# Kernel tuning notes

Measured on AMD Instinct MI355X. Metric: run time of the kernel, lower is better.

## Reference

```python
import jax, jax.numpy as jnp
import numpy as np

N_NODES = 100000
N_EDGES = 1600000
FEAT = 128
EMB = 32
N_GRAPHS = 512


def gcn_conv(x, W, b, src, dst, deg_inv_sqrt):
    # PyG GCNConv: h = x @ W; propagate with norm = d_i^{-1/2} d_j^{-1/2} over A + I
    h = x @ W  # [N, out]
    norm = deg_inv_sqrt[src] * deg_inv_sqrt[dst]  # [E]
    msg = h[src] * norm[:, None]  # gather + scale
    agg = jax.ops.segment_sum(msg, dst, num_segments=N_NODES)
    # self-loop contribution: norm_ii = d_i^{-1}
    agg = agg + h * (deg_inv_sqrt * deg_inv_sqrt)[:, None]
    return agg + b


def setup_inputs() -> dict:
    key = jax.random.key(0)
    ks = jax.random.split(key, 10)
    x = jax.random.normal(ks[0], (N_NODES, FEAT), dtype=jnp.float32)
    edge_index = jax.random.randint(ks[1], (2, N_EDGES), 0, N_NODES, dtype=jnp.int64)
    batch_index = jnp.sort(jax.random.randint(ks[2], (N_NODES,), 0, N_GRAPHS, dtype=jnp.int64))
    # Glorot-ish init for weights (PyG GCNConv lin has no bias arg here but conv bias exists)
    def glorot(k, fan_in, fan_out):
        s = jnp.sqrt(6.0 / (fan_in + fan_out)).astype(jnp.float32)
        return jax.random.uniform(k, (fan_in, fan_out), jnp.float32, -s, s)
    W1 = glorot(ks[3], FEAT, EMB)
    b1 = jnp.zeros((EMB,), jnp.float32)
    W2 = glorot(ks[4], EMB, EMB)
    b2 = jnp.zeros((EMB,), jnp.float32)
    Wo = glorot(ks[5], EMB, 1)
    bo = jnp.zeros((1,), jnp.float32)
    return {"x": x, "edge_index": edge_index, "batch_index": batch_index,
            "W1": W1, "b1": b1, "W2": W2, "b2": b2, "Wo": Wo, "bo": bo}


def reference(x, edge_index, batch_index, W1, b1, W2, b2, Wo, bo):
    src, dst = edge_index[0], edge_index[1]
    # degree over A + I (edge weights = 1, counted on dst as in PyG)
    deg = jax.ops.segment_sum(jnp.ones((N_EDGES,), x.dtype), dst, num_segments=N_NODES) + 1.0
    deg_inv_sqrt = jax.lax.rsqrt(deg)

    out = jax.nn.relu(gcn_conv(x, W1, b1, src, dst, deg_inv_sqrt))
    out = jax.nn.relu(gcn_conv(out, W2, b2, src, dst, deg_inv_sqrt))

    # global mean pool over graphs
    summed = jax.ops.segment_sum(out, batch_index, num_segments=N_GRAPHS)  # [G, EMB]
    counts = jax.ops.segment_sum(jnp.ones((N_NODES,), x.dtype), batch_index, num_segments=N_GRAPHS)
    pooled = summed / jnp.maximum(counts, 1.0)[:, None]

    return pooled @ Wo + bo  # [G, 1]
```

## Files before the change

### kernel.cpp

```cpp
#include <hip/hip_runtime.h>
#include <hip/hip_fp16.h>

#define N_NODES 100000
#define N_EDGES 1600000
#define N_GRAPHS 512
#define FEAT 128
#define EMB 32
#define ZROW N_NODES
#define NCOPY 64
#define NBKT 500
#define NPB 200
#define CAPB 4096
#define COLCAP 5120
#define ABLK 512
#define EPB 3125
#define NTILE (N_NODES / 16)
#define AGB (N_NODES / 32)

typedef unsigned short u16;
typedef unsigned int u32;
typedef _Float16 f16;
typedef float f32x4 __attribute__((ext_vector_type(4)));
typedef unsigned short u16x4 __attribute__((ext_vector_type(4)));
typedef f16 f16x8 __attribute__((ext_vector_type(8)));

__device__ __forceinline__ float4 h4_to_f4(u16x4 v) {
  union { unsigned int u; __half2 h; } a, b;
  a.u = (unsigned int)v.x | ((unsigned int)v.y << 16);
  b.u = (unsigned int)v.z | ((unsigned int)v.w << 16);
  float2 f0 = __half22float2(a.h);
  float2 f1 = __half22float2(b.h);
  return make_float4(f0.x, f0.y, f1.x, f1.y);
}

__device__ __forceinline__ u16x4 f4_to_h4(float4 f) {
  union { unsigned int u; __half2 h; } a, b;
  a.h = __float22half2_rn(make_float2(f.x, f.y));
  b.h = __float22half2_rn(make_float2(f.z, f.w));
  u16x4 r;
  r.x = (u16)(a.u & 0xffff); r.y = (u16)(a.u >> 16);
  r.z = (u16)(b.u & 0xffff); r.w = (u16)(b.u >> 16);
  return r;
}

__device__ __forceinline__ float4 relu_row(float4 acc, float d, float4 bq) {
  float4 o;
  o.x = fmaxf(fmaf(acc.x, d, bq.x), 0.f);
  o.y = fmaxf(fmaf(acc.y, d, bq.y), 0.f);
  o.z = fmaxf(fmaf(acc.z, d, bq.z), 0.f);
  o.w = fmaxf(fmaf(acc.w, d, bq.w), 0.f);
  return o;
}


__global__ __launch_bounds__(256) void k_scat(const int* __restrict__ src,
                                              const int* __restrict__ dst,
                                              int* __restrict__ cur,
                                              u32* __restrict__ binbuf) {
  __shared__ int h[NBKT];
  __shared__ int posB[NBKT];
  int k = blockIdx.x, t = threadIdx.x;
  for (int i = t; i < NBKT; i += 256) h[i] = 0;
  __syncthreads();
  int e0 = k * EPB;
  int e1 = min(e0 + EPB, N_EDGES);
  for (int e = e0 + t; e < e1; e += 256)
    atomicAdd(&h[(u32)dst[e] / (u32)NPB], 1);
  __syncthreads();
  for (int i = t; i < NBKT; i += 256) {
    int c = h[i];
    posB[i] = c ? atomicAdd(&cur[i], c) : 0;
    h[i] = 0;
  }
  __syncthreads();
  for (int e = e0 + t; e < e1; e += 256) {
    u32 d = (u32)dst[e];
    int b = d / (u32)NPB;
    int r = atomicAdd(&h[b], 1);
    binbuf[(size_t)b * CAPB + posB[b] + r] = (u32)src[e] * (u32)NPB + (d - (u32)b * NPB);
  }
}


__global__ __launch_bounds__(256) void k_build(const u32* __restrict__ binbuf,
                                               const int* __restrict__ cur,
                                               int* __restrict__ col,
                                               int2* __restrict__ rowinfo,
                                               float* __restrict__ dis,
                                               u16* __restrict__ hs1) {
  __shared__ int c[NPB];
  __shared__ int sc[256];
  __shared__ int rpl[NPB];
  int b = blockIdx.x, t = threadIdx.x;
  int cnt = cur[b];
  const u32* eb = binbuf + (size_t)b * CAPB;
  for (int i = t; i < NPB; i += 256) c[i] = 0;
  __syncthreads();
  for (int i = t; i < cnt; i += 256) {
    u32 p = eb[i];
    u32 s = p / (u32)NPB;
    atomicAdd(&c[p - s * (u32)NPB], 1);
  }
  __syncthreads();
  int deg = (t < NPB) ? c[t] : 0;
  int p8 = (deg + 7) & ~7;
  sc[t] = p8;
  __syncthreads();
  for (int o = 1; o < 256; o <<= 1) {
    int add = (t >= o) ? sc[t - o] : 0;
    __syncthreads();
    sc[t] += add;
    __syncthreads();
  }
  int colbase = b * COLCAP;
  if (t < NPB) {
    int rp = sc[t] - p8;
    rpl[t] = rp;
    int node = b * NPB + t;
    rowinfo[node] = make_int2(colbase + rp, p8);
    dis[node] = rsqrtf((float)deg + 1.0f);
    for (int j = deg; j < p8; j++) col[colbase + rp + j] = ZROW;
    c[t] = 0;
  }
  __syncthreads();
  for (int i = t; i < cnt; i += 256) {
    u32 p = eb[i];
    u32 s = p / (u32)NPB;
    int ld = (int)(p - s * (u32)NPB);
    int pos = atomicAdd(&c[ld], 1);
    col[colbase + rpl[ld] + pos] = (int)s;
  }
  if (b == 0)
    for (int i = t; i < EMB; i += 256) hs1[(size_t)ZROW * EMB + i] = 0;
}


__global__ __launch_bounds__(256) void k_gemm1(const float* __restrict__ x,
                                               const float* __restrict__ W1,
                                               const float* __restrict__ dis,
                                               u16* __restrict__ hs1) {
  int wid = (blockIdx.x * 256 + threadIdx.x) >> 6;
  if (wid >= NTILE) return;
  int l = threadIdx.x & 63;
  int m = l & 15, q = l >> 4;
  f16x8 B[4][2];
#pragma unroll
  for (int s = 0; s < 4; ++s)
#pragma unroll
    for (int h = 0; h < 2; ++h)
#pragma unroll
      for (int j = 0; j < 8; ++j)
        B[s][h][j] = (f16)W1[(s * 32 + q * 8 + j) * EMB + h * 16 + m];
  int row = wid * 16 + m;
  const float* xr = x + (size_t)row * FEAT + q * 8;
  f32x4 acc0 = {0.f, 0.f, 0.f, 0.f}, acc1 = {0.f, 0.f, 0.f, 0.f};
#pragma unroll
  for (int s = 0; s < 4; ++s) {
    f32x4 xa = __builtin_nontemporal_load((const f32x4*)(xr + s * 32));
    f32x4 xb = __builtin_nontemporal_load((const f32x4*)(xr + s * 32 + 4));
    f16x8 A;
    A[0] = (f16)xa.x; A[1] = (f16)xa.y; A[2] = (f16)xa.z; A[3] = (f16)xa.w;
    A[4] = (f16)xb.x; A[5] = (f16)xb.y; A[6] = (f16)xb.z; A[7] = (f16)xb.w;
    acc0 = __builtin_amdgcn_mfma_f32_16x16x32_f16(A, B[s][0], acc0, 0, 0, 0);
    acc1 = __builtin_amdgcn_mfma_f32_16x16x32_f16(A, B[s][1], acc1, 0, 0, 0);
  }
  f32x4 dq = *(const f32x4*)(dis + wid * 16 + q * 4);
  u16* o = hs1 + (size_t)(wid * 16) * EMB;
#pragma unroll
  for (int i = 0; i < 4; ++i) {
    int r = q * 4 + i;
    float dv = (i == 0) ? dq.x : (i == 1) ? dq.y : (i == 2) ? dq.z : dq.w;
    o[(size_t)r * EMB + m]      = __half_as_ushort(__float2half_rn(acc0[i] * dv));
    o[(size_t)r * EMB + 16 + m] = __half_as_ushort(__float2half_rn(acc1[i] * dv));
  }
}

__global__ __launch_bounds__(256) void k_gemm2(const u16* __restrict__ in1,
                                               const float* __restrict__ W2,
                                               const float* __restrict__ dis,
                                               u16* __restrict__ hs2) {
  int wid = (blockIdx.x * 256 + threadIdx.x) >> 6;
  if (wid >= NTILE) return;
  int l = threadIdx.x & 63;
  int m = l & 15, q = l >> 4;
  f16x8 B[2];
#pragma unroll
  for (int h = 0; h < 2; ++h)
#pragma unroll
    for (int j = 0; j < 8; ++j)
      B[h][j] = (f16)W2[(q * 8 + j) * EMB + h * 16 + m];
  int row = wid * 16 + m;
  f16x8 A = *(const f16x8*)(in1 + (size_t)row * EMB + q * 8);
  f32x4 acc0 = {0.f, 0.f, 0.f, 0.f}, acc1 = {0.f, 0.f, 0.f, 0.f};
  acc0 = __builtin_amdgcn_mfma_f32_16x16x32_f16(A, B[0], acc0, 0, 0, 0);
  acc1 = __builtin_amdgcn_mfma_f32_16x16x32_f16(A, B[1], acc1, 0, 0, 0);
  f32x4 dq = *(const f32x4*)(dis + wid * 16 + q * 4);
  u16* o = hs2 + (size_t)(wid * 16) * EMB;
#pragma unroll
  for (int i = 0; i < 4; ++i) {
    int r = q * 4 + i;
    float dv = (i == 0) ? dq.x : (i == 1) ? dq.y : (i == 2) ? dq.z : dq.w;
    o[(size_t)r * EMB + m]      = __half_as_ushort(__float2half_rn(acc0[i] * dv));
    o[(size_t)r * EMB + 16 + m] = __half_as_ushort(__float2half_rn(acc1[i] * dv));
  }
}


__device__ __forceinline__ void acc4(float4& A, u16x4 v) {
  float4 f = h4_to_f4(v);
  A.x += f.x; A.y += f.y; A.z += f.z; A.w += f.w;
}

__device__ __forceinline__ float4 agg_node(const u16* __restrict__ hs,
                                           const int2* __restrict__ rowinfo,
                                           const int* __restrict__ col,
                                           int node, int sub) {
  const u16x4* t4 = (const u16x4*)hs;
  int2 ri = rowinfo[node];
  int a0 = ri.x, na = ri.y;
  const int* cp = col + a0;
  int4 c0 = *(const int4*)cp;
  int4 c1 = *(const int4*)(cp + 4);
  float4 A = make_float4(0.f, 0.f, 0.f, 0.f);
  for (int i = 0; i < na; i += 8) {
    u16x4 v0 = t4[(size_t)c0.x * 8 + sub];
    u16x4 v1 = t4[(size_t)c0.y * 8 + sub];
    u16x4 v2 = t4[(size_t)c0.z * 8 + sub];
    u16x4 v3 = t4[(size_t)c0.w * 8 + sub];
    u16x4 v4 = t4[(size_t)c1.x * 8 + sub];
    u16x4 v5 = t4[(size_t)c1.y * 8 + sub];
    u16x4 v6 = t4[(size_t)c1.z * 8 + sub];
    u16x4 v7 = t4[(size_t)c1.w * 8 + sub];
    if (i + 8 < na) {
      c0 = *(const int4*)(cp + i + 8);
      c1 = *(const int4*)(cp + i + 12);
    }
    acc4(A, v0); acc4(A, v1); acc4(A, v2); acc4(A, v3);
    acc4(A, v4); acc4(A, v5); acc4(A, v6); acc4(A, v7);
  }
  acc4(A, t4[(size_t)node * 8 + sub]);
  return A;
}

__global__ __launch_bounds__(256) void k_agg1(const u16* __restrict__ hs,
                                              const int2* __restrict__ rowinfo,
                                              const int* __restrict__ col,
                                              const float* __restrict__ dis,
                                              const float* __restrict__ b,
                                              u16* __restrict__ out) {
  int t = threadIdx.x;
  int l = t & 63;
  int node = blockIdx.x * 32 + (t >> 6) * 8 + (l >> 3);
  int sub = l & 7;
  float4 A = agg_node(hs, rowinfo, col, node, sub);
  float4 bq = ((const float4*)b)[sub];
  float4 o = relu_row(A, dis[node], bq);
  ((u16x4*)(out + (size_t)node * EMB))[sub] = f4_to_h4(o);
}

__global__ __launch_bounds__(256) void k_agg2pool(const u16* __restrict__ hs,
                                                  const int2* __restrict__ rowinfo,
                                                  const int* __restrict__ col,
                                                  const float* __restrict__ dis,
                                                  const float* __restrict__ b2,
                                                  const float* __restrict__ Wo,
                                                  const int* __restrict__ batch,
                                                  float* __restrict__ gaccP) {
  int t = threadIdx.x;
  int l = t & 63;
  int node = blockIdx.x * 32 + (t >> 6) * 8 + (l >> 3);
  int sub = l & 7;
  float4 A = agg_node(hs, rowinfo, col, node, sub);
  float4 bq = ((const float4*)b2)[sub];
  float4 wq = ((const float4*)Wo)[sub];
  float4 o = relu_row(A, dis[node], bq);
  float p = o.x * wq.x + o.y * wq.y + o.z * wq.z + o.w * wq.w;
  p += __shfl_xor(p, 1);
  p += __shfl_xor(p, 2);
  p += __shfl_xor(p, 4);
  if (sub == 0)
    atomicAdd(&gaccP[(node & (NCOPY - 1)) * N_GRAPHS + batch[node]], p);
}

__global__ __launch_bounds__(256) void k_finalize(const float* __restrict__ gaccP,
                                                  const int* __restrict__ batch,
                                                  const float* __restrict__ bo,
                                                  float* __restrict__ out) {
  int g = blockIdx.x * 256 + threadIdx.x;
  if (g < N_GRAPHS) {
    int lo = 0, hi = N_NODES;
    while (lo < hi) { int mid = (lo + hi) >> 1; if (batch[mid] < g) lo = mid + 1; else hi = mid; }
    int lo1 = lo; hi = N_NODES;
    while (lo < hi) { int mid = (lo + hi) >> 1; if (batch[mid] < g + 1) lo = mid + 1; else hi = mid; }
    int cntg = lo - lo1;
    float s = 0.f;
#pragma unroll 8
    for (int c = 0; c < NCOPY; ++c) s += gaccP[c * N_GRAPHS + g];
    out[g] = s / fmaxf((float)cntg, 1.0f) + bo[0];
  }
}


extern "C" void kernel_launch(void* const* d_in, const int* in_sizes, int n_in,
                              void* d_out, int out_size, void* d_ws, size_t ws_size,
                              hipStream_t stream) {
  const float* x     = (const float*)d_in[0];
  const int*   ei    = (const int*)d_in[1];
  const int*   batch = (const int*)d_in[2];
  const float* W1    = (const float*)d_in[3];
  const float* b1    = (const float*)d_in[4];
  const float* W2    = (const float*)d_in[5];
  const float* b2    = (const float*)d_in[6];
  const float* Wo    = (const float*)d_in[7];
  const float* bo    = (const float*)d_in[8];
  float* out = (float*)d_out;

  const int* src = ei;
  const int* dst = ei + N_EDGES;

  char* w = (char*)d_ws;
  float* gaccP   = (float*)w;  w += (size_t)NCOPY * N_GRAPHS * 4;
  int*   cur     = (int*)w;    w += (size_t)(NBKT + 8) * 4;
  size_t zero_bytes = (size_t)(w - (char*)d_ws);
  u32*   binbuf  = (u32*)w;    w += (size_t)NBKT * CAPB * 4;
  int*   col     = (int*)w;    w += ((size_t)NBKT * COLCAP + 64) * 4;
  int2*  rowinfo = (int2*)w;   w += (size_t)(N_NODES + 8) * 8;
  float* dis     = (float*)w;  w += (size_t)N_NODES * 4;
  u16*   hs1     = (u16*)w;    w += (size_t)(N_NODES + 1) * EMB * 2;
  u16*   out1    = (u16*)w;    w += (size_t)N_NODES * EMB * 2;
  u16*   hs2     = hs1;

  const int GB = (NTILE * 64 + 255) / 256;

  (void)hipMemsetAsync(d_ws, 0, zero_bytes, stream);

  k_scat<<<ABLK, 256, 0, stream>>>(src, dst, cur, binbuf);
  k_build<<<NBKT, 256, 0, stream>>>(binbuf, cur, col, rowinfo, dis, hs1);
  k_gemm1<<<GB, 256, 0, stream>>>(x, W1, dis, hs1);
  k_agg1<<<AGB, 256, 0, stream>>>(hs1, rowinfo, col, dis, b1, out1);
  k_gemm2<<<GB, 256, 0, stream>>>(out1, W2, dis, hs2);
  k_agg2pool<<<AGB, 256, 0, stream>>>(hs2, rowinfo, col, dis, b2, Wo, batch, gaccP);
  k_finalize<<<2, 256, 0, stream>>>(gaccP, batch, bo, out);
}
```

Measured before the change: 233.0 us.

## Reorder layer-2 GCN to aggregate before W2 and drop gemm2 kernel

Uses linearity of the second GCN layer: agg1 now stores relu output pre-scaled by deg^-1/2, and agg2pool aggregates those 32-wide rows first, then multiplies by W2 held in LDS using lane shuffles. This removes the separate gemm2 launch and its full read/write pass over node features. The cost is extra per-node FMA work and shuffles inside the aggregation kernel, plus an fp16 rounding of the pre-scaled features. The edge-scatter launch config also changes: four times as many blocks with a quarter of the edges per block.

```diff
diff --git a/kernel.cpp b/kernel.cpp
--- a/kernel.cpp
+++ b/kernel.cpp
@@ -12,10 +12,10 @@
 #define NPB 200
 #define CAPB 4096
 #define COLCAP 5120
-#define ABLK 512
-#define EPB 3125
+#define ABLK 2048
+#define EPB 782
 #define NTILE (N_NODES / 16)
-#define AGB (N_NODES / 32)
+#define AGB 3125
 
 typedef unsigned short u16;
 typedef unsigned int u32;
@@ -166,36 +166,6 @@
   }
   f32x4 dq = *(const f32x4*)(dis + wid * 16 + q * 4);
   u16* o = hs1 + (size_t)(wid * 16) * EMB;
-#pragma unroll
-  for (int i = 0; i < 4; ++i) {
-    int r = q * 4 + i;
-    float dv = (i == 0) ? dq.x : (i == 1) ? dq.y : (i == 2) ? dq.z : dq.w;
-    o[(size_t)r * EMB + m]      = __half_as_ushort(__float2half_rn(acc0[i] * dv));
-    o[(size_t)r * EMB + 16 + m] = __half_as_ushort(__float2half_rn(acc1[i] * dv));
-  }
-}
-
-__global__ __launch_bounds__(256) void k_gemm2(const u16* __restrict__ in1,
-                                               const float* __restrict__ W2,
-                                               const float* __restrict__ dis,
-                                               u16* __restrict__ hs2) {
-  int wid = (blockIdx.x * 256 + threadIdx.x) >> 6;
-  if (wid >= NTILE) return;
-  int l = threadIdx.x & 63;
-  int m = l & 15, q = l >> 4;
-  f16x8 B[2];
-#pragma unroll
-  for (int h = 0; h < 2; ++h)
-#pragma unroll
-    for (int j = 0; j < 8; ++j)
-      B[h][j] = (f16)W2[(q * 8 + j) * EMB + h * 16 + m];
-  int row = wid * 16 + m;
-  f16x8 A = *(const f16x8*)(in1 + (size_t)row * EMB + q * 8);
-  f32x4 acc0 = {0.f, 0.f, 0.f, 0.f}, acc1 = {0.f, 0.f, 0.f, 0.f};
-  acc0 = __builtin_amdgcn_mfma_f32_16x16x32_f16(A, B[0], acc0, 0, 0, 0);
-  acc1 = __builtin_amdgcn_mfma_f32_16x16x32_f16(A, B[1], acc1, 0, 0, 0);
-  f32x4 dq = *(const f32x4*)(dis + wid * 16 + q * 4);
-  u16* o = hs2 + (size_t)(wid * 16) * EMB;
 #pragma unroll
   for (int i = 0; i < 4; ++i) {
     int r = q * 4 + i;
@@ -253,8 +223,10 @@
   int node = blockIdx.x * 32 + (t >> 6) * 8 + (l >> 3);
   int sub = l & 7;
   float4 A = agg_node(hs, rowinfo, col, node, sub);
+  float d = dis[node];
   float4 bq = ((const float4*)b)[sub];
-  float4 o = relu_row(A, dis[node], bq);
+  float4 o = relu_row(A, d, bq);
+  o.x *= d; o.y *= d; o.z *= d; o.w *= d;
   ((u16x4*)(out + (size_t)node * EMB))[sub] = f4_to_h4(o);
 }
 
@@ -262,18 +234,40 @@
                                                   const int2* __restrict__ rowinfo,
                                                   const int* __restrict__ col,
                                                   const float* __restrict__ dis,
+                                                  const float* __restrict__ W2,
                                                   const float* __restrict__ b2,
                                                   const float* __restrict__ Wo,
                                                   const int* __restrict__ batch,
                                                   float* __restrict__ gaccP) {
+  __shared__ float W2L[32][32];
   int t = threadIdx.x;
+  for (int i = t; i < 32 * 32; i += 256) ((float*)W2L)[i] = W2[i];
+  __syncthreads();
   int l = t & 63;
   int node = blockIdx.x * 32 + (t >> 6) * 8 + (l >> 3);
   int sub = l & 7;
   float4 A = agg_node(hs, rowinfo, col, node, sub);
+  int base = l & ~7;
+  float4 z = make_float4(0.f, 0.f, 0.f, 0.f);
+#pragma unroll
+  for (int s8 = 0; s8 < 8; ++s8) {
+    float sx = __shfl(A.x, base + s8);
+    float sy = __shfl(A.y, base + s8);
+    float sz = __shfl(A.z, base + s8);
+    float sw = __shfl(A.w, base + s8);
+    float4 w0 = *(const float4*)&W2L[4 * s8 + 0][sub * 4];
+    float4 w1 = *(const float4*)&W2L[4 * s8 + 1][sub * 4];
+    float4 w2 = *(const float4*)&W2L[4 * s8 + 2][sub * 4];
+    float4 w3 = *(const float4*)&W2L[4 * s8 + 3][sub * 4];
+    z.x = fmaf(sx, w0.x, fmaf(sy, w1.x, fmaf(sz, w2.x, fmaf(sw, w3.x, z.x))));
+    z.y = fmaf(sx, w0.y, fmaf(sy, w1.y, fmaf(sz, w2.y, fmaf(sw, w3.y, z.y))));
+    z.z = fmaf(sx, w0.z, fmaf(sy, w1.z, fmaf(sz, w2.z, fmaf(sw, w3.z, z.z))));
+    z.w = fmaf(sx, w0.w, fmaf(sy, w1.w, fmaf(sz, w2.w, fmaf(sw, w3.w, z.w))));
+  }
+  float d = dis[node];
   float4 bq = ((const float4*)b2)[sub];
+  float4 o = relu_row(z, d, bq);
   float4 wq = ((const float4*)Wo)[sub];
-  float4 o = relu_row(A, dis[node], bq);
   float p = o.x * wq.x + o.y * wq.y + o.z * wq.z + o.w * wq.w;
   p += __shfl_xor(p, 1);
   p += __shfl_xor(p, 2);
@@ -327,18 +321,17 @@
   int2*  rowinfo = (int2*)w;   w += (size_t)(N_NODES + 8) * 8;
   float* dis     = (float*)w;  w += (size_t)N_NODES * 4;
   u16*   hs1     = (u16*)w;    w += (size_t)(N_NODES + 1) * EMB * 2;
-  u16*   out1    = (u16*)w;    w += (size_t)N_NODES * EMB * 2;
-  u16*   hs2     = hs1;
+  u16*   out1    = (u16*)w;    w += (size_t)(N_NODES + 1) * EMB * 2;
 
   const int GB = (NTILE * 64 + 255) / 256;
 
   (void)hipMemsetAsync(d_ws, 0, zero_bytes, stream);
+  (void)hipMemsetAsync(out1 + (size_t)ZROW * EMB, 0, EMB * 2, stream);
 
   k_scat<<<ABLK, 256, 0, stream>>>(src, dst, cur, binbuf);
   k_build<<<NBKT, 256, 0, stream>>>(binbuf, cur, col, rowinfo, dis, hs1);
   k_gemm1<<<GB, 256, 0, stream>>>(x, W1, dis, hs1);
   k_agg1<<<AGB, 256, 0, stream>>>(hs1, rowinfo, col, dis, b1, out1);
-  k_gemm2<<<GB, 256, 0, stream>>>(out1, W2, dis, hs2);
-  k_agg2pool<<<AGB, 256, 0, stream>>>(hs2, rowinfo, col, dis, b2, Wo, batch, gaccP);
+  k_agg2pool<<<AGB, 256, 0, stream>>>(out1, rowinfo, col, dis, W2, b2, Wo, batch, gaccP);
   k_finalize<<<2, 256, 0, stream>>>(gaccP, batch, bo, out);
 }
```

After: 272.8 us. +17.1%, slower.
